# Performance work log

Measured on AMD Instinct MI355X. Metric: run time of the kernel, lower is better.

Reference implementation:

```python
import jax, jax.numpy as jnp
import numpy as np

S, D, H, E = 4096, 1024, 16, 64  # seq_len, embed_dim, n_heads, head_size


def setup_inputs() -> dict:
    key = jax.random.key(0)
    ks = jax.random.split(key, 8)
    s_d = 1.0 / np.sqrt(D).astype(np.float32)
    return {
        "x": jax.random.normal(ks[0], (S, D), jnp.float32),
        # per-head Q/K/V projections (no bias), stacked over heads: [H, D, E]
        "Wk": jax.random.normal(ks[1], (H, D, E), jnp.float32) * s_d,
        "Wq": jax.random.normal(ks[2], (H, D, E), jnp.float32) * s_d,
        "Wv": jax.random.normal(ks[3], (H, D, E), jnp.float32) * s_d,
        # output projection Dense(D) with bias
        "Wo": jax.random.normal(ks[4], (H * E, D), jnp.float32) * (1.0 / np.sqrt(H * E).astype(np.float32)),
        "bo": jnp.zeros((D,), jnp.float32),
        # MLP: Dense(4D) -> gelu -> Dense(D), both with bias
        "W1": jax.random.normal(ks[5], (D, 4 * D), jnp.float32) * s_d,
        "b1": jnp.zeros((4 * D,), jnp.float32),
        "W2": jax.random.normal(ks[6], (4 * D, D), jnp.float32) * (1.0 / np.sqrt(4 * D).astype(np.float32)),
        "b2": jnp.zeros((D,), jnp.float32),
    }


def _attention(x, Wk, Wq, Wv):
    # per-head projections, vectorized over heads (original loops in Python)
    k = jnp.einsum('sd,hde->hse', x, Wk)
    q = jnp.einsum('sd,hde->hse', x, Wq)
    v = jnp.einsum('sd,hde->hse', x, Wv)
    # NOTE: original computes keys @ queries.T -> scores[i, j] = k_i . q_j
    scores = jnp.einsum('hse,hte->hst', k, q) / jnp.sqrt(jnp.float32(E))
    mask = jnp.tril(jnp.ones((x.shape[0], x.shape[0]), dtype=bool))  # [S, S]
    w = jax.nn.softmax(jnp.where(mask, scores, -jnp.inf), axis=-1)   # [H, S, S]
    out = jnp.einsum('hst,hte->hse', w, v)                            # [H, S, E]
    # concatenate heads along feature axis (head 0 first, matching the loop)
    return out.transpose(1, 0, 2).reshape(x.shape[0], -1)             # [S, H*E]


def reference(x, Wk, Wq, Wv, Wo, bo, W1, b1, W2, b2):
    x = x + _attention(x, Wk, Wq, Wv) @ Wo + bo
    h = jax.nn.gelu(x @ W1 + b1, approximate=True)  # flax default gelu (tanh approx)
    return x + h @ W2 + b2
```

## Files before the change

### kernel.cpp

```cpp
#include <hip/hip_runtime.h>

typedef __attribute__((ext_vector_type(8))) short s16x8;
typedef __attribute__((ext_vector_type(4))) short s16x4;
typedef __attribute__((ext_vector_type(4))) float f32x4;


__device__ __forceinline__ unsigned short f2bf(float f) {
    union { float f; unsigned u; } v; v.f = f;
    unsigned r = v.u + 0x7FFFu + ((v.u >> 16) & 1u);
    return (unsigned short)(r >> 16);
}

__device__ __forceinline__ float bf2f(unsigned short b) {
    union { unsigned u; float f; } v; v.u = ((unsigned)b) << 16;
    return v.f;
}

__device__ __forceinline__ unsigned cvt_pk_bf16(float lo, float hi) {
    unsigned r;
    asm("v_cvt_pk_bf16_f32 %0, %1, %2" : "=v"(r) : "v"(lo), "v"(hi));
    return r;
}

__device__ __forceinline__ float exp2_fast(float x) {
    float r;
    asm("v_exp_f32 %0, %1" : "=v"(r) : "v"(x));
    return r;
}

__device__ __forceinline__ float gelu_tanh(float x) {
    float u = 0.7978845608028654f * (x + 0.044715f * x * x * x);
    float au = fabsf(u);
    float t = 1.f - 2.f / (__expf(2.f * au) + 1.f);
    t = (u < 0.f) ? -t : t;
    return 0.5f * x * (1.f + t);
}

__device__ __forceinline__ void load_lds16(const void* g, void* l) {
    __builtin_amdgcn_global_load_lds(
        (const __attribute__((address_space(1))) void*)g,
        (__attribute__((address_space(3))) void*)l, 16, 0, 0);
}

__device__ __forceinline__ void xcd_remap(int& bx, int& by) {
    const int gx = gridDim.x;
    const int nwg = gx * gridDim.y;
    const int id = by * gx + bx;
    const int nid = (id & 7) * (nwg >> 3) + (id >> 3);
    bx = nid % gx; by = nid / gx;
}


__global__ void convert_bf16_k(const float* __restrict__ in,
                               unsigned short* __restrict__ out, int n) {
    int i = (blockIdx.x * blockDim.x + threadIdx.x) * 4;
    if (i >= n) return;
    float4 v = *(const float4*)(in + i);
    ushort4 o;
    o.x = f2bf(v.x); o.y = f2bf(v.y); o.z = f2bf(v.z); o.w = f2bf(v.w);
    *(ushort4*)(out + i) = o;
}

__global__ void transpose_k(const float* __restrict__ in,
                            unsigned short* __restrict__ out, int R, int C) {
    __shared__ float tile[32][33];
    const int b = blockIdx.z;
    const int c0 = blockIdx.x * 32, r0 = blockIdx.y * 32;
    const float* inb = in + (size_t)b * R * C;
    unsigned short* outb = out + (size_t)b * R * C;
    const int tx = threadIdx.x, ty = threadIdx.y;
    #pragma unroll
    for (int i = 0; i < 4; ++i)
        tile[ty + i*8][tx] = inb[(size_t)(r0 + ty + i*8) * C + c0 + tx];
    __syncthreads();
    #pragma unroll
    for (int i = 0; i < 4; ++i)
        outb[(size_t)(c0 + ty + i*8) * R + r0 + tx] = f2bf(tile[tx][ty + i*8]);
}

template<int EPI>
__global__ __launch_bounds__(256) void gemm_bt(
    const unsigned short* __restrict__ A,
    const unsigned short* __restrict__ BT,
    const float* __restrict__ bias,
    const float* __restrict__ resid,
    float* __restrict__ Cf,
    unsigned short* __restrict__ Cb,
    int M, int N, int K)
{
    __shared__ unsigned short As[3][128 * 32];
    __shared__ unsigned short Bs[3][128 * 32];
    const int tid = threadIdx.x;
    const int w  = tid >> 6, l = tid & 63;
    const int wr = w >> 1,  wc = w & 1;
    const int lg = l >> 4,  ll = l & 15;
    int bx = blockIdx.x, by = blockIdx.y;
    xcd_remap(bx, by);
    const int m0 = by * 128, n0 = bx * 128;

    const int srow = w * 16 + (l >> 2);
    const int scol = (((l & 3) ^ ((l >> 2) & 3))) * 8;

    f32x4 acc[4][4] = {};

    auto stage = [&](int buf, int k0) {
        #pragma unroll
        for (int i = 0; i < 2; ++i) {
            load_lds16(A  + (size_t)(m0 + srow + i*64) * K + k0 + scol,
                       (char*)As[buf] + i*4096 + w*1024);
            load_lds16(BT + (size_t)(n0 + srow + i*64) * K + k0 + scol,
                       (char*)Bs[buf] + i*4096 + w*1024);
        }
    };

    const int nsteps = K >> 5;
    stage(0, 0); stage(1, 32);
    int buf = 0;
    for (int s = 0; s < nsteps; ++s) {
        if (s + 1 < nsteps) asm volatile("s_waitcnt vmcnt(4)" ::: "memory");
        else                asm volatile("s_waitcnt vmcnt(0)" ::: "memory");
        __builtin_amdgcn_s_barrier();
        s16x8 a[4], b[4];
        #pragma unroll
        for (int m = 0; m < 4; ++m) {
            const int row = wr*64 + m*16 + ll;
            a[m] = *(const s16x8*)&As[buf][row * 32 + ((lg ^ (ll & 3)) * 8)];
        }
        #pragma unroll
        for (int n = 0; n < 4; ++n) {
            const int row = wc*64 + n*16 + ll;
            b[n] = *(const s16x8*)&Bs[buf][row * 32 + ((lg ^ (ll & 3)) * 8)];
        }
        int bnext = buf + 2; if (bnext >= 3) bnext -= 3;
        if (s + 2 < nsteps) stage(bnext, (s + 2) << 5);
        __builtin_amdgcn_s_setprio(1);
        #pragma unroll
        for (int m = 0; m < 4; ++m)
            #pragma unroll
            for (int n = 0; n < 4; ++n)
                acc[m][n] = __builtin_amdgcn_mfma_f32_16x16x32_bf16(a[m], b[n], acc[m][n], 0, 0, 0);
        __builtin_amdgcn_s_setprio(0);
        buf = (buf == 2) ? 0 : buf + 1;
    }

    #pragma unroll
    for (int m = 0; m < 4; ++m) {
        #pragma unroll
        for (int n = 0; n < 4; ++n) {
            const int col = n0 + wc*64 + n*16 + ll;
            #pragma unroll
            for (int r = 0; r < 4; ++r) {
                const int row = m0 + wr*64 + m*16 + lg*4 + r;
                float v = acc[m][n][r];
                if constexpr (EPI == 2) v = gelu_tanh(v + bias[col]);
                if constexpr (EPI == 4) v *= (col < 1024) ? 0.1803368801f : 1.0f;
                Cb[(size_t)row * N + col] = f2bf(v);
            }
        }
    }
}

template<int EPI>
__global__ __launch_bounds__(256) void gemm_bt64(
    const unsigned short* __restrict__ A,
    const unsigned short* __restrict__ BT,
    const float* __restrict__ bias,
    const float* __restrict__ resid,
    float* __restrict__ Cf,
    unsigned short* __restrict__ Cb,
    int M, int N, int K)
{
    __shared__ unsigned short As[4][128 * 32];
    __shared__ unsigned short Bs[4][64 * 32];
    const int tid = threadIdx.x;
    const int w  = tid >> 6, l = tid & 63;
    const int lg = l >> 4,  ll = l & 15;
    int bx = blockIdx.x, by = blockIdx.y;
    xcd_remap(bx, by);
    const int m0 = by * 128, n0 = bx * 64;

    const int srowA = w * 16 + (l >> 2);
    const int scolA = (((l & 3) ^ ((l >> 2) & 3))) * 8;
    const int srowB = tid >> 2;
    const int scolB = (((tid & 3) ^ ((tid >> 2) & 3))) * 8;

    f32x4 acc[2][4] = {};

    auto stage = [&](int buf, int k0) {
        #pragma unroll
        for (int i = 0; i < 2; ++i)
            load_lds16(A + (size_t)(m0 + srowA + i*64) * K + k0 + scolA,
                       (char*)As[buf] + i*4096 + w*1024);
        load_lds16(BT + (size_t)(n0 + srowB) * K + k0 + scolB,
                   (char*)Bs[buf] + w*1024);
    };

    const int nsteps = K >> 5;
    stage(0, 0); stage(1, 32); stage(2, 64);
    int buf = 0;
    for (int s = 0; s < nsteps; ++s) {
        const int rem = nsteps - 1 - s;
        if (rem >= 2)      asm volatile("s_waitcnt vmcnt(6)" ::: "memory");
        else if (rem == 1) asm volatile("s_waitcnt vmcnt(3)" ::: "memory");
        else               asm volatile("s_waitcnt vmcnt(0)" ::: "memory");
        __builtin_amdgcn_s_barrier();
        s16x8 a[2], b[4];
        #pragma unroll
        for (int m = 0; m < 2; ++m) {
            const int row = w*32 + m*16 + ll;
            a[m] = *(const s16x8*)&As[buf][row * 32 + ((lg ^ (ll & 3)) * 8)];
        }
        #pragma unroll
        for (int n = 0; n < 4; ++n) {
            const int row = n*16 + ll;
            b[n] = *(const s16x8*)&Bs[buf][row * 32 + ((lg ^ (ll & 3)) * 8)];
        }
        int bnext = buf + 3; if (bnext >= 4) bnext -= 4;
        if (s + 3 < nsteps) stage(bnext, (s + 3) << 5);
        __builtin_amdgcn_s_setprio(1);
        #pragma unroll
        for (int m = 0; m < 2; ++m)
            #pragma unroll
            for (int n = 0; n < 4; ++n)
                acc[m][n] = __builtin_amdgcn_mfma_f32_16x16x32_bf16(a[m], b[n], acc[m][n], 0, 0, 0);
        __builtin_amdgcn_s_setprio(0);
        buf = (buf + 1) & 3;
    }

    #pragma unroll
    for (int m = 0; m < 2; ++m) {
        #pragma unroll
        for (int n = 0; n < 4; ++n) {
            const int col = n0 + n*16 + ll;
            #pragma unroll
            for (int r = 0; r < 4; ++r) {
                const int row = m0 + w*32 + m*16 + lg*4 + r;
                float v = acc[m][n][r];
                if constexpr (EPI == 1 || EPI == 3) v += bias[col] + resid[(size_t)row * N + col];
                if constexpr (EPI != 3)
                    Cb[(size_t)row * N + col] = f2bf(v);
                if constexpr (EPI == 1 || EPI == 3)
                    Cf[(size_t)row * N + col] = v;
            }
        }
    }
}

__global__ __launch_bounds__(256) void attn_k(
    const unsigned short* __restrict__ Rq,
    const unsigned short* __restrict__ Ck,
    const unsigned short* __restrict__ Vt,
    unsigned short* __restrict__ Ppart,
    float* __restrict__ Lpart)
{
    __shared__ unsigned short Ks[3][64 * 64];
    __shared__ unsigned short Vs[3][64 * 64];

    const int bx = blockIdx.x;
    const int h  = bx & 15;
    const int j  = (bx >> 4) & 1;
    const int sb = 31 - (bx >> 5);
    const int t0 = j ? (sb + 1) : 0;
    const int t1 = j ? (2*sb + 2) : (sb + 1);

    const int tid = threadIdx.x;
    const int w = tid >> 6, l = tid & 63;
    const int lg = l >> 4, ll = l & 15;

    const int gsrc  = ((l & 7) ^ (l >> 3)) * 8;
    const int kOff0 = (w*16 +     (l >> 3)) * 2048 + h*64 + gsrc;
    const int kOff1 = (w*16 + 8 + (l >> 3)) * 2048 + h*64 + gsrc;
    const int vOff0 = (h*64 + w*16 +     (l >> 3)) * 4096 + gsrc;
    const int vOff1 = (h*64 + w*16 + 8 + (l >> 3)) * 4096 + gsrc;
    const int ldsOff = w * 2048;

    int qkoff[4][2];
    #pragma unroll
    for (int jj = 0; jj < 4; ++jj) {
        const int row = jj*16 + ll, r7 = row & 7;
        qkoff[jj][0] = row*128 + ((lg)     ^ r7) * 16;
        qkoff[jj][1] = row*128 + ((4 + lg) ^ r7) * 16;
    }
    int pvoff[4][2][2];
    #pragma unroll
    for (int n = 0; n < 4; ++n) {
        const int row = n*16 + ll, r7 = row & 7;
        #pragma unroll
        for (int c = 0; c < 2; ++c) {
            const int gl = (c*4     + (lg >> 1)) ^ r7;
            const int gh = (c*4 + 2 + (lg >> 1)) ^ r7;
            pvoff[n][c][0] = row*128 + gl*16 + (lg & 1)*8;
            pvoff[n][c][1] = row*128 + gh*16 + (lg & 1)*8;
        }
    }

    auto stage = [&](int t, int buf) {
        const unsigned short* qsrc = Ck + (size_t)t * 131072;
        const unsigned short* vsrc = Vt + t * 64;
        char* kd = (char*)Ks[buf] + ldsOff;
        char* vd = (char*)Vs[buf] + ldsOff;
        load_lds16(qsrc + kOff0, kd);
        load_lds16(qsrc + kOff1, kd + 1024);
        load_lds16(vsrc + vOff0, vd);
        load_lds16(vsrc + vOff1, vd + 1024);
    };

    const int row0 = sb*128 + w*32;
    const int qgA  = row0 + ll;
    const int qgB  = row0 + 16 + ll;
    const size_t rbA = (size_t)qgA * 2048 + h*64;
    const size_t rbB = (size_t)qgB * 2048 + h*64;
    const s16x8 rA0 = *(const s16x8*)&Rq[rbA + lg*8];
    const s16x8 rA1 = *(const s16x8*)&Rq[rbA + 32 + lg*8];
    const s16x8 rB0 = *(const s16x8*)&Rq[rbB + lg*8];
    const s16x8 rB1 = *(const s16x8*)&Rq[rbB + 32 + lg*8];

    const short onebf = (short)0x3F80;
    const s16x8 ones = {onebf, onebf, onebf, onebf, onebf, onebf, onebf, onebf};

    f32x4 o[2][4] = {};
    f32x4 o4[2] = {};

    stage(t0, 0);
    if (t0 + 1 < t1) stage(t0 + 1, 1);
    int buf = 0;

    for (int t = t0; t < t1; ++t) {
        if (t < t1-1) asm volatile("s_waitcnt vmcnt(4)" ::: "memory");
        else          asm volatile("s_waitcnt vmcnt(0)" ::: "memory");
        __builtin_amdgcn_s_barrier();
        const char* kb = (const char*)Ks[buf];
        const char* vb = (const char*)Vs[buf];
        const bool diag = (t >= 2*sb);

        f32x4 st[2][4];
        __builtin_amdgcn_s_setprio(1);
        #pragma unroll
        for (int jj = 0; jj < 4; ++jj) {
            s16x8 k0 = *(const s16x8*)(kb + qkoff[jj][0]);
            s16x8 k1 = *(const s16x8*)(kb + qkoff[jj][1]);
            f32x4 z = {0.f, 0.f, 0.f, 0.f};
            f32x4 ta = __builtin_amdgcn_mfma_f32_16x16x32_bf16(k0, rA0, z, 0, 0, 0);
            st[0][jj] = __builtin_amdgcn_mfma_f32_16x16x32_bf16(k1, rA1, ta, 0, 0, 0);
            f32x4 tb = __builtin_amdgcn_mfma_f32_16x16x32_bf16(k0, rB0, z, 0, 0, 0);
            st[1][jj] = __builtin_amdgcn_mfma_f32_16x16x32_bf16(k1, rB1, tb, 0, 0, 0);
        }
        __builtin_amdgcn_s_setprio(0);

        int bnext = buf + 2; if (bnext >= 3) bnext -= 3;
        if (t + 2 < t1) stage(t + 2, bnext);

        float p[2][4][4];
        if (diag) {
            #pragma unroll
            for (int jj = 0; jj < 4; ++jj)
                #pragma unroll
                for (int r = 0; r < 4; ++r) {
                    const int jg = t*64 + jj*16 + lg*4 + r;
                    p[0][jj][r] = exp2_fast((jg > qgA) ? -3e38f : st[0][jj][r]);
                    p[1][jj][r] = exp2_fast((jg > qgB) ? -3e38f : st[1][jj][r]);
                }
        } else {
            #pragma unroll
            for (int rs = 0; rs < 2; ++rs)
                #pragma unroll
                for (int jj = 0; jj < 4; ++jj)
                    #pragma unroll
                    for (int r = 0; r < 4; ++r)
                        p[rs][jj][r] = exp2_fast(st[rs][jj][r]);
        }

        s16x8 apv[2][2];
        #pragma unroll
        for (int rs = 0; rs < 2; ++rs)
            #pragma unroll
            for (int c = 0; c < 2; ++c) {
                union { unsigned u[4]; s16x8 v; } pk;
                pk.u[0] = cvt_pk_bf16(p[rs][2*c][0],   p[rs][2*c][1]);
                pk.u[1] = cvt_pk_bf16(p[rs][2*c][2],   p[rs][2*c][3]);
                pk.u[2] = cvt_pk_bf16(p[rs][2*c+1][0], p[rs][2*c+1][1]);
                pk.u[3] = cvt_pk_bf16(p[rs][2*c+1][2], p[rs][2*c+1][3]);
                apv[rs][c] = pk.v;
            }
        __builtin_amdgcn_s_setprio(1);
        #pragma unroll
        for (int rs = 0; rs < 2; ++rs) {
            o4[rs] = __builtin_amdgcn_mfma_f32_16x16x32_bf16(apv[rs][0], ones, o4[rs], 0, 0, 0);
            o4[rs] = __builtin_amdgcn_mfma_f32_16x16x32_bf16(apv[rs][1], ones, o4[rs], 0, 0, 0);
        }
        #pragma unroll
        for (int n = 0; n < 4; ++n) {
            #pragma unroll
            for (int c = 0; c < 2; ++c) {
                s16x4 lo = *(const s16x4*)(vb + pvoff[n][c][0]);
                s16x4 hi = *(const s16x4*)(vb + pvoff[n][c][1]);
                union { s16x4 h2[2]; s16x8 v; } u;
                u.h2[0] = lo; u.h2[1] = hi;
                o[0][n] = __builtin_amdgcn_mfma_f32_16x16x32_bf16(apv[0][c], u.v, o[0][n], 0, 0, 0);
                o[1][n] = __builtin_amdgcn_mfma_f32_16x16x32_bf16(apv[1][c], u.v, o[1][n], 0, 0, 0);
            }
        }
        __builtin_amdgcn_s_setprio(0);

        buf = (buf == 2) ? 0 : buf + 1;
    }

    unsigned short* Pout = Ppart + (size_t)j * 4194304;
    float* Lout = Lpart + (size_t)j * 65536;
    #pragma unroll
    for (int rs = 0; rs < 2; ++rs)
        #pragma unroll
        for (int r = 0; r < 4; ++r) {
            const int row = row0 + rs*16 + lg*4 + r;
            const size_t orow = (size_t)row * 1024 + h * 64;
            #pragma unroll
            for (int n = 0; n < 4; ++n)
                Pout[orow + n*16 + ll] = f2bf(o[rs][n][r]);
            if (ll == 0) Lout[row * 16 + h] = o4[rs][r];
        }
}

__global__ __launch_bounds__(256) void attn_combine_k(
    const unsigned short* __restrict__ P,
    const float* __restrict__ L,
    unsigned short* __restrict__ Out)
{
    const int idx = (blockIdx.x * 256 + threadIdx.x) * 4;
    const int row = idx >> 10, h = (idx & 1023) >> 6;
    const float inv = 1.f / (L[row*16 + h] + L[65536 + row*16 + h]);
    ushort4 a = *(const ushort4*)(P + idx);
    ushort4 b = *(const ushort4*)(P + 4194304 + idx);
    ushort4 o;
    o.x = f2bf((bf2f(a.x) + bf2f(b.x)) * inv);
    o.y = f2bf((bf2f(a.y) + bf2f(b.y)) * inv);
    o.z = f2bf((bf2f(a.z) + bf2f(b.z)) * inv);
    o.w = f2bf((bf2f(a.w) + bf2f(b.w)) * inv);
    *(ushort4*)(Out + idx) = o;
}


extern "C" void kernel_launch(void* const* d_in, const int* in_sizes, int n_in,
                              void* d_out, int out_size, void* d_ws, size_t ws_size,
                              hipStream_t stream) {
    const float* x  = (const float*)d_in[0];
    const float* Wk = (const float*)d_in[1];
    const float* Wq = (const float*)d_in[2];
    const float* Wv = (const float*)d_in[3];
    const float* Wo = (const float*)d_in[4];
    const float* bo = (const float*)d_in[5];
    const float* W1 = (const float*)d_in[6];
    const float* b1 = (const float*)d_in[7];
    const float* W2 = (const float*)d_in[8];
    const float* b2 = (const float*)d_in[9];
    float* out = (float*)d_out;

    char* ws = (char*)d_ws;
    unsigned short* x_bf  = (unsigned short*)(ws);
    unsigned short* WqkT  = (unsigned short*)(ws + (8u  << 20));
    unsigned short* WvT   = (unsigned short*)(ws + (12u << 20));
    unsigned short* WoT   = (unsigned short*)(ws + (14u << 20));
    unsigned short* W1T   = (unsigned short*)(ws + (16u << 20));
    unsigned short* W2T   = (unsigned short*)(ws + (24u << 20));
    unsigned short* QKm   = (unsigned short*)(ws + (32u << 20));
    unsigned short* attn  = (unsigned short*)(ws + (48u << 20));
    unsigned short* Vt    = (unsigned short*)(ws + (56u << 20));
    float*          yf    = (float*)(ws + (64u << 20));
    float*          Lpart = (float*)ws;
    unsigned short* Ppart = (unsigned short*)(ws + (64u << 20));
    unsigned short* y_bf  = x_bf;
    unsigned short* h_bf  = QKm;

    dim3 tb(32, 8);
    convert_bf16_k<<<4096, 256, 0, stream>>>(x, x_bf, 4096 * 1024);
    transpose_k<<<dim3(2, 32, 16),  tb, 0, stream>>>(Wq, WqkT,               1024, 64);
    transpose_k<<<dim3(2, 32, 16),  tb, 0, stream>>>(Wk, WqkT + 1024 * 1024, 1024, 64);
    transpose_k<<<dim3(2, 32, 16),  tb, 0, stream>>>(Wv, WvT, 1024, 64);
    transpose_k<<<dim3(32, 32, 1),  tb, 0, stream>>>(Wo, WoT, 1024, 1024);
    transpose_k<<<dim3(128, 32, 1), tb, 0, stream>>>(W1, W1T, 1024, 4096);
    transpose_k<<<dim3(32, 128, 1), tb, 0, stream>>>(W2, W2T, 4096, 1024);

    gemm_bt<4><<<dim3(16, 32), 256, 0, stream>>>(x_bf, WqkT, nullptr, nullptr, nullptr,
                                                 QKm, 4096, 2048, 1024);
    gemm_bt64<0><<<dim3(64, 8), 256, 0, stream>>>(WvT, x_bf, nullptr, nullptr, nullptr,
                                                  Vt, 1024, 4096, 1024);

    attn_k<<<1024, 256, 0, stream>>>(QKm + 1024 , QKm , Vt, Ppart, Lpart);
    attn_combine_k<<<4096, 256, 0, stream>>>(Ppart, Lpart, attn);

    gemm_bt64<1><<<dim3(16, 32), 256, 0, stream>>>(attn, WoT, bo, x, yf, y_bf, 4096, 1024, 1024);
    gemm_bt<2><<<dim3(32, 32),   256, 0, stream>>>(y_bf, W1T, b1, nullptr, nullptr, h_bf, 4096, 4096, 1024);
    gemm_bt64<3><<<dim3(16, 32), 256, 0, stream>>>(h_bf, W2T, b2, yf, out, nullptr, 4096, 1024, 4096);
}
```

Baseline: 251.8 us.

## Split-K the MLP down-projection, retile QK GEMM, and unroll attention buffers

The W2 GEMM is split along K into two halves over blockIdx.z. Each half writes bf16 partials, and a new combine kernel adds them with bias and residual to form the fp32 output. The aim is to fill more CUs than the 512-tile grid could. The QK projection moves from the 128x128 gemm_bt to the 128x64 gemm_bt64 with a larger grid, and gemm_bt64 drops from four LDS stages to three. The attention loop is manually unrolled by three so buffer indices are compile-time constants. Costs: an extra kernel launch, a bf16 rounding of the partial sums, and a shallower prefetch depth in gemm_bt64.

```diff
diff --git a/kernel.cpp b/kernel.cpp
--- a/kernel.cpp
+++ b/kernel.cpp
@@ -153,7 +153,6 @@
                 const int row = m0 + wr*64 + m*16 + lg*4 + r;
                 float v = acc[m][n][r];
                 if constexpr (EPI == 2) v = gelu_tanh(v + bias[col]);
-                if constexpr (EPI == 4) v *= (col < 1024) ? 0.1803368801f : 1.0f;
                 Cb[(size_t)row * N + col] = f2bf(v);
             }
         }
@@ -168,16 +167,18 @@
     const float* __restrict__ resid,
     float* __restrict__ Cf,
     unsigned short* __restrict__ Cb,
-    int M, int N, int K)
+    int M, int N, int K, int klen)
 {
-    __shared__ unsigned short As[4][128 * 32];
-    __shared__ unsigned short Bs[4][64 * 32];
+    __shared__ unsigned short As[3][128 * 32];
+    __shared__ unsigned short Bs[3][64 * 32];
     const int tid = threadIdx.x;
     const int w  = tid >> 6, l = tid & 63;
     const int lg = l >> 4,  ll = l & 15;
     int bx = blockIdx.x, by = blockIdx.y;
     xcd_remap(bx, by);
     const int m0 = by * 128, n0 = bx * 64;
+    const int kh = (EPI == 5) ? (int)blockIdx.z : 0;
+    const int koff = kh * klen;
 
     const int srowA = w * 16 + (l >> 2);
     const int scolA = (((l & 3) ^ ((l >> 2) & 3))) * 8;
@@ -189,20 +190,18 @@
     auto stage = [&](int buf, int k0) {
         #pragma unroll
         for (int i = 0; i < 2; ++i)
-            load_lds16(A + (size_t)(m0 + srowA + i*64) * K + k0 + scolA,
+            load_lds16(A + (size_t)(m0 + srowA + i*64) * K + koff + k0 + scolA,
                        (char*)As[buf] + i*4096 + w*1024);
-        load_lds16(BT + (size_t)(n0 + srowB) * K + k0 + scolB,
+        load_lds16(BT + (size_t)(n0 + srowB) * K + koff + k0 + scolB,
                    (char*)Bs[buf] + w*1024);
     };
 
-    const int nsteps = K >> 5;
-    stage(0, 0); stage(1, 32); stage(2, 64);
+    const int nsteps = klen >> 5;
+    stage(0, 0); stage(1, 32);
     int buf = 0;
     for (int s = 0; s < nsteps; ++s) {
-        const int rem = nsteps - 1 - s;
-        if (rem >= 2)      asm volatile("s_waitcnt vmcnt(6)" ::: "memory");
-        else if (rem == 1) asm volatile("s_waitcnt vmcnt(3)" ::: "memory");
-        else               asm volatile("s_waitcnt vmcnt(0)" ::: "memory");
+        if (s + 1 < nsteps) asm volatile("s_waitcnt vmcnt(3)" ::: "memory");
+        else                asm volatile("s_waitcnt vmcnt(0)" ::: "memory");
         __builtin_amdgcn_s_barrier();
         s16x8 a[2], b[4];
         #pragma unroll
@@ -215,8 +214,8 @@
             const int row = n*16 + ll;
             b[n] = *(const s16x8*)&Bs[buf][row * 32 + ((lg ^ (ll & 3)) * 8)];
         }
-        int bnext = buf + 3; if (bnext >= 4) bnext -= 4;
-        if (s + 3 < nsteps) stage(bnext, (s + 3) << 5);
+        int bnext = buf + 2; if (bnext >= 3) bnext -= 3;
+        if (s + 2 < nsteps) stage(bnext, (s + 2) << 5);
         __builtin_amdgcn_s_setprio(1);
         #pragma unroll
         for (int m = 0; m < 2; ++m)
@@ -224,9 +223,10 @@
             for (int n = 0; n < 4; ++n)
                 acc[m][n] = __builtin_amdgcn_mfma_f32_16x16x32_bf16(a[m], b[n], acc[m][n], 0, 0, 0);
         __builtin_amdgcn_s_setprio(0);
-        buf = (buf + 1) & 3;
-    }
-
+        buf = (buf == 2) ? 0 : buf + 1;
+    }
+
+    unsigned short* Cbz = (EPI == 5) ? (Cb + (size_t)kh * M * N) : Cb;
     #pragma unroll
     for (int m = 0; m < 2; ++m) {
         #pragma unroll
@@ -236,14 +236,33 @@
             for (int r = 0; r < 4; ++r) {
                 const int row = m0 + w*32 + m*16 + lg*4 + r;
                 float v = acc[m][n][r];
-                if constexpr (EPI == 1 || EPI == 3) v += bias[col] + resid[(size_t)row * N + col];
-                if constexpr (EPI != 3)
-                    Cb[(size_t)row * N + col] = f2bf(v);
-                if constexpr (EPI == 1 || EPI == 3)
+                if constexpr (EPI == 1) v += bias[col] + resid[(size_t)row * N + col];
+                if constexpr (EPI == 4) v *= (col < 1024) ? 0.1803368801f : 1.0f;
+                Cbz[(size_t)row * N + col] = f2bf(v);
+                if constexpr (EPI == 1)
                     Cf[(size_t)row * N + col] = v;
             }
         }
     }
+}
+
+__global__ __launch_bounds__(256) void mlp2_combine_k(
+    const unsigned short* __restrict__ P,
+    const float* __restrict__ bias,
+    const float* __restrict__ resid,
+    float* __restrict__ out)
+{
+    const int idx = (blockIdx.x * 256 + threadIdx.x) * 4;
+    const int col = idx & 1023;
+    ushort4 a = *(const ushort4*)(P + idx);
+    ushort4 b = *(const ushort4*)(P + 4194304 + idx);
+    float4 rs = *(const float4*)(resid + idx);
+    float4 o;
+    o.x = bf2f(a.x) + bf2f(b.x) + bias[col]     + rs.x;
+    o.y = bf2f(a.y) + bf2f(b.y) + bias[col + 1] + rs.y;
+    o.z = bf2f(a.z) + bf2f(b.z) + bias[col + 2] + rs.z;
+    o.w = bf2f(a.w) + bf2f(b.w) + bias[col + 3] + rs.w;
+    *(float4*)(out + idx) = o;
 }
 
 __global__ __launch_bounds__(256) void attn_k(
@@ -294,15 +313,13 @@
         }
     }
 
-    auto stage = [&](int t, int buf) {
+    auto stageTo = [&](int t, char* kd, char* vd) {
         const unsigned short* qsrc = Ck + (size_t)t * 131072;
         const unsigned short* vsrc = Vt + t * 64;
-        char* kd = (char*)Ks[buf] + ldsOff;
-        char* vd = (char*)Vs[buf] + ldsOff;
-        load_lds16(qsrc + kOff0, kd);
-        load_lds16(qsrc + kOff1, kd + 1024);
-        load_lds16(vsrc + vOff0, vd);
-        load_lds16(vsrc + vOff1, vd + 1024);
+        load_lds16(qsrc + kOff0, kd + ldsOff);
+        load_lds16(qsrc + kOff1, kd + ldsOff + 1024);
+        load_lds16(vsrc + vOff0, vd + ldsOff);
+        load_lds16(vsrc + vOff1, vd + ldsOff + 1024);
     };
 
     const int row0 = sb*128 + w*32;
@@ -321,16 +338,15 @@
     f32x4 o[2][4] = {};
     f32x4 o4[2] = {};
 
-    stage(t0, 0);
-    if (t0 + 1 < t1) stage(t0 + 1, 1);
-    int buf = 0;
-
-    for (int t = t0; t < t1; ++t) {
-        if (t < t1-1) asm volatile("s_waitcnt vmcnt(4)" ::: "memory");
-        else          asm volatile("s_waitcnt vmcnt(0)" ::: "memory");
+    const int cnt = t1 - t0;
+    stageTo(t0, (char*)Ks[0], (char*)Vs[0]);
+    if (cnt > 1) stageTo(t0 + 1, (char*)Ks[1], (char*)Vs[1]);
+
+    auto tileBody = [&](int t, const char* kb, const char* vb,
+                        char* kd, char* vd, bool last) {
+        if (!last) asm volatile("s_waitcnt vmcnt(4)" ::: "memory");
+        else       asm volatile("s_waitcnt vmcnt(0)" ::: "memory");
         __builtin_amdgcn_s_barrier();
-        const char* kb = (const char*)Ks[buf];
-        const char* vb = (const char*)Vs[buf];
         const bool diag = (t >= 2*sb);
 
         f32x4 st[2][4];
@@ -347,8 +363,7 @@
         }
         __builtin_amdgcn_s_setprio(0);
 
-        int bnext = buf + 2; if (bnext >= 3) bnext -= 3;
-        if (t + 2 < t1) stage(t + 2, bnext);
+        if (t + 2 < t1) stageTo(t + 2, kd, vd);
 
         float p[2][4][4];
         if (diag) {
@@ -401,8 +416,22 @@
             }
         }
         __builtin_amdgcn_s_setprio(0);
-
-        buf = (buf == 2) ? 0 : buf + 1;
+    };
+
+    const int nfull = cnt - 1;
+    int i = 0;
+    for (; i + 3 <= nfull; i += 3) {
+        tileBody(t0+i,   (const char*)Ks[0], (const char*)Vs[0], (char*)Ks[2], (char*)Vs[2], false);
+        tileBody(t0+i+1, (const char*)Ks[1], (const char*)Vs[1], (char*)Ks[0], (char*)Vs[0], false);
+        tileBody(t0+i+2, (const char*)Ks[2], (const char*)Vs[2], (char*)Ks[1], (char*)Vs[1], false);
+    }
+    for (; i < nfull; ++i) {
+        const int b = i % 3, b2 = (i + 2) % 3;
+        tileBody(t0+i, (const char*)Ks[b], (const char*)Vs[b], (char*)Ks[b2], (char*)Vs[b2], false);
+    }
+    {
+        const int b = nfull % 3, b2 = (nfull + 2) % 3;
+        tileBody(t0+nfull, (const char*)Ks[b], (const char*)Vs[b], (char*)Ks[b2], (char*)Vs[b2], true);
     }
 
     unsigned short* Pout = Ppart + (size_t)j * 4194304;
@@ -467,6 +496,7 @@
     float*          yf    = (float*)(ws + (64u << 20));
     float*          Lpart = (float*)ws;
     unsigned short* Ppart = (unsigned short*)(ws + (64u << 20));
+    unsigned short* Pmlp  = (unsigned short*)(ws);
     unsigned short* y_bf  = x_bf;
     unsigned short* h_bf  = QKm;
 
@@ -479,15 +509,19 @@
     transpose_k<<<dim3(128, 32, 1), tb, 0, stream>>>(W1, W1T, 1024, 4096);
     transpose_k<<<dim3(32, 128, 1), tb, 0, stream>>>(W2, W2T, 4096, 1024);
 
-    gemm_bt<4><<<dim3(16, 32), 256, 0, stream>>>(x_bf, WqkT, nullptr, nullptr, nullptr,
-                                                 QKm, 4096, 2048, 1024);
+    gemm_bt64<4><<<dim3(32, 32), 256, 0, stream>>>(x_bf, WqkT, nullptr, nullptr, nullptr,
+                                                   QKm, 4096, 2048, 1024, 1024);
     gemm_bt64<0><<<dim3(64, 8), 256, 0, stream>>>(WvT, x_bf, nullptr, nullptr, nullptr,
-                                                  Vt, 1024, 4096, 1024);
+                                                  Vt, 1024, 4096, 1024, 1024);
 
     attn_k<<<1024, 256, 0, stream>>>(QKm + 1024 , QKm , Vt, Ppart, Lpart);
     attn_combine_k<<<4096, 256, 0, stream>>>(Ppart, Lpart, attn);
 
-    gemm_bt64<1><<<dim3(16, 32), 256, 0, stream>>>(attn, WoT, bo, x, yf, y_bf, 4096, 1024, 1024);
-    gemm_bt<2><<<dim3(32, 32),   256, 0, stream>>>(y_bf, W1T, b1, nullptr, nullptr, h_bf, 4096, 4096, 1024);
-    gemm_bt64<3><<<dim3(16, 32), 256, 0, stream>>>(h_bf, W2T, b2, yf, out, nullptr, 4096, 1024, 4096);
-}
+    gemm_bt64<1><<<dim3(16, 32), 256, 0, stream>>>(attn, WoT, bo, x, yf, y_bf,
+                                                   4096, 1024, 1024, 1024);
+    gemm_bt<2><<<dim3(32, 32), 256, 0, stream>>>(y_bf, W1T, b1, nullptr, nullptr, h_bf,
+                                                 4096, 4096, 1024);
+    gemm_bt64<5><<<dim3(16, 32, 2), 256, 0, stream>>>(h_bf, W2T, nullptr, nullptr, nullptr,
+                                                      Pmlp, 4096, 1024, 4096, 2048);
+    mlp2_combine_k<<<4096, 256, 0, stream>>>(Pmlp, b2, yf, out);
+}
```

Result: slower. 260.6 us (+3.5%).
